# Performance work log

Hardware: AMD Instinct MI355X
Metric: run time of the kernel (lower is better)

Reference implementation:

```python
import jax, jax.numpy as jnp
import numpy as np

N = 131072          # number of input points
M = 512             # num_prototypes
D = 64              # feature_dim
GAMMA = 1.0


def setup_inputs() -> dict:
    key = jax.random.key(0)
    kx, kp = jax.random.split(key)
    x = jax.random.normal(kx, (N, D), dtype=jnp.float32)
    prototypes = jax.random.normal(kp, (M, D), dtype=jnp.float32)
    return {"x": x, "prototypes": prototypes}


def reference(x, prototypes):
    x_sq = jnp.sum(x * x, axis=-1, keepdims=True)            # [N, 1]
    p_sq = jnp.sum(prototypes * prototypes, axis=-1)         # [M]
    cross = jnp.einsum('nd,md->nm', x, prototypes)           # [N, M]
    dist2 = x_sq + p_sq[None, :] - 2.0 * cross               # [N, M]
    dist2 = jnp.maximum(dist2, 0.0)                          # guard tiny negatives
    return jnp.exp(-GAMMA * dist2)
```

## Files before the change

### kernel.cpp

```cpp
#include <hip/hip_runtime.h>
#include <hip/hip_bf16.h>


#define N_PTS 131072
#define M_PROT 512
#define D_DIM 64
#define BN 128
#define BM 128
#define LDP 72

typedef __attribute__((ext_vector_type(8))) short short8;
typedef __attribute__((ext_vector_type(4))) float f32x4;

__device__ inline ushort f2bf(float f) {
  uint u = __float_as_uint(f);
  uint r = (u + 0x7FFFu + ((u >> 16) & 1u)) >> 16;
  return (ushort)r;
}
__device__ inline float bf2f(ushort h) { return __uint_as_float(((uint)h) << 16); }

__device__ inline void split4(float4 v, uint2& hp, uint2& lp) {
  ushort h0 = f2bf(v.x), h1 = f2bf(v.y), h2 = f2bf(v.z), h3 = f2bf(v.w);
  ushort l0 = f2bf(v.x - bf2f(h0));
  ushort l1 = f2bf(v.y - bf2f(h1));
  ushort l2 = f2bf(v.z - bf2f(h2));
  ushort l3 = f2bf(v.w - bf2f(h3));
  hp.x = (uint)h0 | ((uint)h1 << 16);
  hp.y = (uint)h2 | ((uint)h3 << 16);
  lp.x = (uint)l0 | ((uint)l1 << 16);
  lp.y = (uint)l2 | ((uint)l3 << 16);
}

__global__ __launch_bounds__(256, 2)
void rbf_mfma(const float* __restrict__ x,
              const float* __restrict__ prot,
              float* __restrict__ out) {
  __shared__ ushort XH[BN][LDP], XL[BN][LDP];
  __shared__ ushort PH[BM][LDP], PL[BM][LDP];
  __shared__ float XS[BN], PS[BM];

  const int tid = threadIdx.x;
  const int bid = blockIdx.x;
  const int n0 = (bid >> 2) * BN;
  const int m0 = (bid & 3) * BM;

#pragma unroll
  for (int i = 0; i < 8; ++i) {
    const int idx = tid + i * 256;
    const int r = idx >> 4;
    const int c4 = idx & 15;
    const float4 v = *reinterpret_cast<const float4*>(x + (size_t)(n0 + r) * D_DIM + c4 * 4);
    uint2 hp, lp;
    split4(v, hp, lp);
    *reinterpret_cast<uint2*>(&XH[r][c4 * 4]) = hp;
    *reinterpret_cast<uint2*>(&XL[r][c4 * 4]) = lp;
  }
#pragma unroll
  for (int i = 0; i < 8; ++i) {
    const int idx = tid + i * 256;
    const int r = idx >> 4;
    const int c4 = idx & 15;
    const float4 v = *reinterpret_cast<const float4*>(prot + (size_t)(m0 + r) * D_DIM + c4 * 4);
    uint2 hp, lp;
    split4(v, hp, lp);
    *reinterpret_cast<uint2*>(&PH[r][c4 * 4]) = hp;
    *reinterpret_cast<uint2*>(&PL[r][c4 * 4]) = lp;
  }

  {
    const int r = tid & 127;
    const float* src = (tid < 128) ? (x + (size_t)(n0 + r) * D_DIM)
                                   : (prot + (size_t)(m0 + r) * D_DIM);
    float s = 0.f;
#pragma unroll
    for (int c = 0; c < 16; ++c) {
      const float4 v = *reinterpret_cast<const float4*>(src + c * 4);
      s = fmaf(v.x, v.x, s);
      s = fmaf(v.y, v.y, s);
      s = fmaf(v.z, v.z, s);
      s = fmaf(v.w, v.w, s);
    }
    if (tid < 128) XS[r] = s; else PS[r] = s;
  }
  __syncthreads();

  const int lane = tid & 63;
  const int wave = tid >> 6;
  const int wr = wave >> 1, wc = wave & 1;
  const int lrow = lane & 15;
  const int kg16 = (lane >> 4) * 8;

  f32x4 acc[4][4];
#pragma unroll
  for (int i = 0; i < 4; ++i)
#pragma unroll
    for (int j = 0; j < 4; ++j)
      acc[i][j] = (f32x4){0.f, 0.f, 0.f, 0.f};

#pragma unroll
  for (int s = 0; s < 3; ++s) {
    const ushort(*A)[LDP] = (s == 2) ? XL : XH;
    const ushort(*B)[LDP] = (s == 1) ? PL : PH;
#pragma unroll
    for (int h = 0; h < 2; ++h) {
      const int d0 = h * 32 + kg16;
      short8 a[4], b[4];
#pragma unroll
      for (int f = 0; f < 4; ++f) {
        a[f] = *reinterpret_cast<const short8*>(&A[wr * 64 + f * 16 + lrow][d0]);
        b[f] = *reinterpret_cast<const short8*>(&B[wc * 64 + f * 16 + lrow][d0]);
      }
#pragma unroll
      for (int i = 0; i < 4; ++i)
#pragma unroll
        for (int j = 0; j < 4; ++j)
          acc[i][j] = __builtin_amdgcn_mfma_f32_16x16x32_bf16(a[i], b[j], acc[i][j], 0, 0, 0);
      }
  }

  const int rloc = wr * 64 + (lane >> 4) * 4;
  const int cloc = wc * 64 + (lane & 15);
#pragma unroll
  for (int i = 0; i < 4; ++i) {
#pragma unroll
    for (int j = 0; j < 4; ++j) {
      const f32x4 c = acc[i][j];
      const int col = cloc + j * 16;
      const float psv = PS[col];
      float* outp = out + (size_t)(n0 + rloc + i * 16) * M_PROT + (m0 + col);
#pragma unroll
      for (int r = 0; r < 4; ++r) {
        const float xsv = XS[rloc + i * 16 + r];
        const float e = fminf(fmaf(2.f, c[r], -xsv) - psv, 0.f);
        outp[(size_t)r * M_PROT] = __expf(e);
      }
    }
  }
}

extern "C" void kernel_launch(void* const* d_in, const int* in_sizes, int n_in,
                              void* d_out, int out_size, void* d_ws, size_t ws_size,
                              hipStream_t stream) {
  const float* x = (const float*)d_in[0];
  const float* p = (const float*)d_in[1];
  float* out = (float*)d_out;
  (void)in_sizes; (void)n_in; (void)out_size; (void)d_ws; (void)ws_size;
  rbf_mfma<<<dim3((N_PTS / BN) * (M_PROT / BM)), 256, 0, stream>>>(x, p, out);
}
```

Before: 342.7 us.

## Load MFMA fragments directly from global, drop LDS, transpose output for float4 stores

Removes the shared-memory staging and barrier. Each wave loads its bf16 hi/lo fragments straight from global memory, splitting by truncation instead of rounding, and computes norms with lane shuffles. Operands are swapped so the accumulator layout lets each lane write a contiguous float4 of output, replacing scalar strided stores. It also adds an XCD-aware block remap and raises occupancy to 3 blocks per CU. The cost is duplicated global loads across waves and a slightly different hi/lo split precision.

```diff
diff --git a/kernel.cpp b/kernel.cpp
--- a/kernel.cpp
+++ b/kernel.cpp
@@ -1,139 +1,119 @@
 #include <hip/hip_runtime.h>
-#include <hip/hip_bf16.h>
 
 
 #define N_PTS 131072
 #define M_PROT 512
 #define D_DIM 64
-#define BN 128
-#define BM 128
-#define LDP 72
 
 typedef __attribute__((ext_vector_type(8))) short short8;
 typedef __attribute__((ext_vector_type(4))) float f32x4;
 
-__device__ inline ushort f2bf(float f) {
-  uint u = __float_as_uint(f);
-  uint r = (u + 0x7FFFu + ((u >> 16) & 1u)) >> 16;
-  return (ushort)r;
-}
-__device__ inline float bf2f(ushort h) { return __uint_as_float(((uint)h) << 16); }
+union FragU { uint u[4]; short8 s; };
 
-__device__ inline void split4(float4 v, uint2& hp, uint2& lp) {
-  ushort h0 = f2bf(v.x), h1 = f2bf(v.y), h2 = f2bf(v.z), h3 = f2bf(v.w);
-  ushort l0 = f2bf(v.x - bf2f(h0));
-  ushort l1 = f2bf(v.y - bf2f(h1));
-  ushort l2 = f2bf(v.z - bf2f(h2));
-  ushort l3 = f2bf(v.w - bf2f(h3));
-  hp.x = (uint)h0 | ((uint)h1 << 16);
-  hp.y = (uint)h2 | ((uint)h3 << 16);
-  lp.x = (uint)l0 | ((uint)l1 << 16);
-  lp.y = (uint)l2 | ((uint)l3 << 16);
+__device__ inline void load_split(const float* p, short8& hi, short8& lo, float& nrm) {
+  const float4 a = *reinterpret_cast<const float4*>(p);
+  const float4 b = *reinterpret_cast<const float4*>(p + 4);
+  const float f[8] = {a.x, a.y, a.z, a.w, b.x, b.y, b.z, b.w};
+  FragU H, L;
+#pragma unroll
+  for (int i = 0; i < 4; ++i) {
+    const uint u0 = __float_as_uint(f[2 * i]);
+    const uint u1 = __float_as_uint(f[2 * i + 1]);
+    H.u[i] = (u0 >> 16) | (u1 & 0xFFFF0000u);
+    const float l0 = f[2 * i]     - __uint_as_float(u0 & 0xFFFF0000u);
+    const float l1 = f[2 * i + 1] - __uint_as_float(u1 & 0xFFFF0000u);
+    L.u[i] = (__float_as_uint(l0) >> 16) | (__float_as_uint(l1) & 0xFFFF0000u);
+    nrm = fmaf(f[2 * i], f[2 * i], nrm);
+    nrm = fmaf(f[2 * i + 1], f[2 * i + 1], nrm);
+  }
+  hi = H.s;
+  lo = L.s;
 }
 
-__global__ __launch_bounds__(256, 2)
+__global__ __launch_bounds__(256, 3)
 void rbf_mfma(const float* __restrict__ x,
               const float* __restrict__ prot,
               float* __restrict__ out) {
-  __shared__ ushort XH[BN][LDP], XL[BN][LDP];
-  __shared__ ushort PH[BM][LDP], PL[BM][LDP];
-  __shared__ float XS[BN], PS[BM];
+  const int tid = threadIdx.x;
+  const int lane = tid & 63;
+  const int w = tid >> 6;
 
-  const int tid = threadIdx.x;
   const int bid = blockIdx.x;
-  const int n0 = (bid >> 2) * BN;
-  const int m0 = (bid & 3) * BM;
+  const int wg = (bid & 7) * 512 + (bid >> 3);
+  const int ntile = wg >> 2;
+  const int mtile = wg & 3;
+  const int n0w = ntile * 128 + (w >> 1) * 64;
+  const int m0w = mtile * 128 + (w & 1) * 64;
 
-#pragma unroll
-  for (int i = 0; i < 8; ++i) {
-    const int idx = tid + i * 256;
-    const int r = idx >> 4;
-    const int c4 = idx & 15;
-    const float4 v = *reinterpret_cast<const float4*>(x + (size_t)(n0 + r) * D_DIM + c4 * 4);
-    uint2 hp, lp;
-    split4(v, hp, lp);
-    *reinterpret_cast<uint2*>(&XH[r][c4 * 4]) = hp;
-    *reinterpret_cast<uint2*>(&XL[r][c4 * 4]) = lp;
-  }
-#pragma unroll
-  for (int i = 0; i < 8; ++i) {
-    const int idx = tid + i * 256;
-    const int r = idx >> 4;
-    const int c4 = idx & 15;
-    const float4 v = *reinterpret_cast<const float4*>(prot + (size_t)(m0 + r) * D_DIM + c4 * 4);
-    uint2 hp, lp;
-    split4(v, hp, lp);
-    *reinterpret_cast<uint2*>(&PH[r][c4 * 4]) = hp;
-    *reinterpret_cast<uint2*>(&PL[r][c4 * 4]) = lp;
-  }
-
-  {
-    const int r = tid & 127;
-    const float* src = (tid < 128) ? (x + (size_t)(n0 + r) * D_DIM)
-                                   : (prot + (size_t)(m0 + r) * D_DIM);
-    float s = 0.f;
-#pragma unroll
-    for (int c = 0; c < 16; ++c) {
-      const float4 v = *reinterpret_cast<const float4*>(src + c * 4);
-      s = fmaf(v.x, v.x, s);
-      s = fmaf(v.y, v.y, s);
-      s = fmaf(v.z, v.z, s);
-      s = fmaf(v.w, v.w, s);
-    }
-    if (tid < 128) XS[r] = s; else PS[r] = s;
-  }
-  __syncthreads();
-
-  const int lane = tid & 63;
-  const int wave = tid >> 6;
-  const int wr = wave >> 1, wc = wave & 1;
-  const int lrow = lane & 15;
-  const int kg16 = (lane >> 4) * 8;
+  const int lr = lane & 15;
+  const int kg = (lane >> 4) * 8;
 
   f32x4 acc[4][4];
 #pragma unroll
   for (int i = 0; i < 4; ++i)
 #pragma unroll
-    for (int j = 0; j < 4; ++j)
-      acc[i][j] = (f32x4){0.f, 0.f, 0.f, 0.f};
+    for (int j = 0; j < 4; ++j) acc[i][j] = (f32x4){0.f, 0.f, 0.f, 0.f};
+
+  float ps_part[4] = {0.f, 0.f, 0.f, 0.f};
+  float xs_part[4] = {0.f, 0.f, 0.f, 0.f};
 
 #pragma unroll
-  for (int s = 0; s < 3; ++s) {
-    const ushort(*A)[LDP] = (s == 2) ? XL : XH;
-    const ushort(*B)[LDP] = (s == 1) ? PL : PH;
+  for (int h = 0; h < 2; ++h) {
+    short8 PH[4], PL[4], XH[4], XL[4];
 #pragma unroll
-    for (int h = 0; h < 2; ++h) {
-      const int d0 = h * 32 + kg16;
-      short8 a[4], b[4];
+    for (int fi = 0; fi < 4; ++fi) {
+      const float* src = prot + (size_t)(m0w + fi * 16 + lr) * D_DIM + h * 32 + kg;
+      load_split(src, PH[fi], PL[fi], ps_part[fi]);
+    }
 #pragma unroll
-      for (int f = 0; f < 4; ++f) {
-        a[f] = *reinterpret_cast<const short8*>(&A[wr * 64 + f * 16 + lrow][d0]);
-        b[f] = *reinterpret_cast<const short8*>(&B[wc * 64 + f * 16 + lrow][d0]);
-      }
+    for (int fj = 0; fj < 4; ++fj) {
+      const float* src = x + (size_t)(n0w + fj * 16 + lr) * D_DIM + h * 32 + kg;
+      load_split(src, XH[fj], XL[fj], xs_part[fj]);
+    }
 #pragma unroll
-      for (int i = 0; i < 4; ++i)
+    for (int fi = 0; fi < 4; ++fi)
 #pragma unroll
-        for (int j = 0; j < 4; ++j)
-          acc[i][j] = __builtin_amdgcn_mfma_f32_16x16x32_bf16(a[i], b[j], acc[i][j], 0, 0, 0);
-      }
+      for (int fj = 0; fj < 4; ++fj)
+        acc[fi][fj] = __builtin_amdgcn_mfma_f32_16x16x32_bf16(PH[fi], XH[fj], acc[fi][fj], 0, 0, 0);
+#pragma unroll
+    for (int fi = 0; fi < 4; ++fi)
+#pragma unroll
+      for (int fj = 0; fj < 4; ++fj)
+        acc[fi][fj] = __builtin_amdgcn_mfma_f32_16x16x32_bf16(PH[fi], XL[fj], acc[fi][fj], 0, 0, 0);
+#pragma unroll
+    for (int fi = 0; fi < 4; ++fi)
+#pragma unroll
+      for (int fj = 0; fj < 4; ++fj)
+        acc[fi][fj] = __builtin_amdgcn_mfma_f32_16x16x32_bf16(PL[fi], XH[fj], acc[fi][fj], 0, 0, 0);
   }
 
-  const int rloc = wr * 64 + (lane >> 4) * 4;
-  const int cloc = wc * 64 + (lane & 15);
 #pragma unroll
-  for (int i = 0; i < 4; ++i) {
+  for (int f = 0; f < 4; ++f) {
+    ps_part[f] += __shfl_xor(ps_part[f], 16);
+    ps_part[f] += __shfl_xor(ps_part[f], 32);
+    xs_part[f] += __shfl_xor(xs_part[f], 16);
+    xs_part[f] += __shfl_xor(xs_part[f], 32);
+  }
+  f32x4 psv[4];
 #pragma unroll
-    for (int j = 0; j < 4; ++j) {
-      const f32x4 c = acc[i][j];
-      const int col = cloc + j * 16;
-      const float psv = PS[col];
-      float* outp = out + (size_t)(n0 + rloc + i * 16) * M_PROT + (m0 + col);
+  for (int fi = 0; fi < 4; ++fi)
 #pragma unroll
-      for (int r = 0; r < 4; ++r) {
-        const float xsv = XS[rloc + i * 16 + r];
-        const float e = fminf(fmaf(2.f, c[r], -xsv) - psv, 0.f);
-        outp[(size_t)r * M_PROT] = __expf(e);
-      }
+    for (int r = 0; r < 4; ++r)
+      psv[fi][r] = __shfl(ps_part[fi], (lane >> 4) * 4 + r);
+
+#pragma unroll
+  for (int fi = 0; fi < 4; ++fi) {
+#pragma unroll
+    for (int fj = 0; fj < 4; ++fj) {
+      const f32x4 c = acc[fi][fj];
+      const float xsv = xs_part[fj];
+      float4 e;
+      e.x = __expf(fminf(fmaf(2.f, c[0], -xsv) - psv[fi][0], 0.f));
+      e.y = __expf(fminf(fmaf(2.f, c[1], -xsv) - psv[fi][1], 0.f));
+      e.z = __expf(fminf(fmaf(2.f, c[2], -xsv) - psv[fi][2], 0.f));
+      e.w = __expf(fminf(fmaf(2.f, c[3], -xsv) - psv[fi][3], 0.f));
+      float* addr = out + (size_t)(n0w + fj * 16 + lr) * M_PROT + m0w + fi * 16 + (lane >> 4) * 4;
+      *reinterpret_cast<float4*>(addr) = e;
     }
   }
 }
@@ -145,5 +125,5 @@
   const float* p = (const float*)d_in[1];
   float* out = (float*)d_out;
   (void)in_sizes; (void)n_in; (void)out_size; (void)d_ws; (void)ws_size;
-  rbf_mfma<<<dim3((N_PTS / BN) * (M_PROT / BM)), 256, 0, stream>>>(x, p, out);
+  rbf_mfma<<<(N_PTS / 128) * (M_PROT / 128), 256, 0, stream>>>(x, p, out);
 }
```

Measured after the change: 381.0 us. 11.2% more time.
